# Performance work log

Measured on AMD Instinct MI355X. Metric: run time of the kernel, lower is better.

## Reference

```python
import jax, jax.numpy as jnp
import numpy as np

EPS = 1e-5

def group_norm(x, gamma, beta, groups):
    b, c, h, w = x.shape
    xg = x.reshape(b, groups, c // groups, h, w)
    mean = xg.mean(axis=(2, 3, 4), keepdims=True)
    var = xg.var(axis=(2, 3, 4), keepdims=True)
    xg = (xg - mean) * jax.lax.rsqrt(var + EPS)
    x = xg.reshape(b, c, h, w)
    return x * gamma[None, :, None, None] + beta[None, :, None, None]

def setup_inputs() -> dict:
    key = jax.random.key(0)
    ks = jax.random.split(key, 7)
    b, c, h, w = 8, 256, 64, 64
    x = jax.random.normal(ks[0], (b, c, h, w), dtype=jnp.float32)
    # GroupNorm affine params
    gamma = jnp.ones((c,), dtype=jnp.float32)
    beta = jnp.zeros((c,), dtype=jnp.float32)
    # 1x1 convs == linear maps over channel dim
    s = 1.0 / np.sqrt(c)
    w_qkv = jax.random.uniform(ks[1], (3 * c, c), jnp.float32, -s, s)
    b_qkv = jax.random.uniform(ks[2], (3 * c,), jnp.float32, -s, s)
    w_proj = jax.random.uniform(ks[3], (c, c), jnp.float32, -s, s)
    b_proj = jax.random.uniform(ks[4], (c,), jnp.float32, -s, s)
    return {"x": x, "gamma": gamma, "beta": beta, "w_qkv": w_qkv,
            "b_qkv": b_qkv, "w_proj": w_proj, "b_proj": b_proj}

def reference(x, gamma, beta, w_qkv, b_qkv, w_proj, b_proj):
    b, c, h, w = x.shape
    n = h * w
    h_in = x
    xn = group_norm(x, gamma, beta, groups=8)
    # 1x1 conv qkv: [b,c,h,w] -> [b,3c,h,w] -> [b,3c,n]
    qkv = jnp.einsum('oc,bchw->bohw', w_qkv, xn) + b_qkv[None, :, None, None]
    qkv = qkv.reshape(b, 3 * c, n)
    q, k, v = jnp.split(qkv, 3, axis=1)          # each [b,c,n]
    # attn = softmax(q^T k / sqrt(c)) over last dim
    scores = jnp.einsum('bci,bcj->bij', q, k) / jnp.sqrt(jnp.float32(c))
    attn = jax.nn.softmax(scores, axis=-1)       # [b,n,n]
    out = jnp.einsum('bij,bcj->bci', attn, v)    # [b,c,n]
    out = out.reshape(b, c, h, w)
    out = jnp.einsum('oc,bchw->bohw', w_proj, out) + b_proj[None, :, None, None]
    return h_in + out
```

## Files before the change

kernel.cpp:

```cpp
#include <hip/hip_runtime.h>
#include <hip/hip_bf16.h>
#include <stdint.h>

typedef __bf16 bf16_t;
typedef __bf16 bf16x8 __attribute__((ext_vector_type(8)));
typedef __bf16 bf16x4 __attribute__((ext_vector_type(4)));
typedef float f32x4 __attribute__((ext_vector_type(4)));
typedef float f32x16 __attribute__((ext_vector_type(16)));

#define NPIX 4096
#define CH 256

__global__ __launch_bounds__(256) void gn_partial_k(const float* __restrict__ x,
                                                    float* __restrict__ acc2) {
  int bg = blockIdx.x >> 3;
  int chunk = blockIdx.x & 7;
  const float4* xp = (const float4*)(x + (size_t)bg * 32 * NPIX) + chunk * (32 * NPIX / 4 / 8);
  float s = 0.f, ss = 0.f;
  for (int i = threadIdx.x; i < 32 * NPIX / 4 / 8; i += 256) {
    float4 v = xp[i];
    s  += v.x + v.y + v.z + v.w;
    ss += v.x * v.x + v.y * v.y + v.z * v.z + v.w * v.w;
  }
  int l = threadIdx.x & 63, w = threadIdx.x >> 6;
  #pragma unroll
  for (int off = 32; off; off >>= 1) { s += __shfl_down(s, off); ss += __shfl_down(ss, off); }
  __shared__ float rs[4], rss[4];
  if (l == 0) { rs[w] = s; rss[w] = ss; }
  __syncthreads();
  if (threadIdx.x == 0) {
    atomicAdd(&acc2[bg * 2],     rs[0] + rs[1] + rs[2] + rs[3]);
    atomicAdd(&acc2[bg * 2 + 1], rss[0] + rss[1] + rss[2] + rss[3]);
  }
}

__global__ void gn_finalize_k(const float* __restrict__ acc2, float* __restrict__ stats) {
  int bg = threadIdx.x;
  float mean = acc2[bg * 2] * (1.f / (32.f * NPIX));
  float var  = acc2[bg * 2 + 1] * (1.f / (32.f * NPIX)) - mean * mean;
  stats[bg * 2]     = mean;
  stats[bg * 2 + 1] = rsqrtf(var + 1e-5f);
}

__global__ __launch_bounds__(256) void gn_apply_t_k(const float* __restrict__ x,
    const float* __restrict__ stats, const float* __restrict__ gamma,
    const float* __restrict__ beta, bf16_t* __restrict__ xnT) {
  __shared__ float tile[32][33];
  int b = blockIdx.z;
  int p0 = blockIdx.x * 32, c0 = blockIdx.y * 32;
  int g = c0 >> 5;
  float mean = stats[(b * 8 + g) * 2], rstd = stats[(b * 8 + g) * 2 + 1];
  int tx = threadIdx.x, ty = threadIdx.y;
  const float* xb = x + ((size_t)b * CH + c0) * NPIX + p0;
  #pragma unroll
  for (int j = 0; j < 4; ++j) {
    int c = ty + j * 8;
    float v = xb[(size_t)c * NPIX + tx];
    tile[c][tx] = (v - mean) * rstd * gamma[c0 + c] + beta[c0 + c];
  }
  __syncthreads();
  bf16_t* op = xnT + ((size_t)b * NPIX + p0) * CH + c0;
  #pragma unroll
  for (int j = 0; j < 4; ++j) {
    int p = ty + j * 8;
    op[(size_t)p * CH + tx] = (bf16_t)tile[tx][p];
  }
}

__global__ __launch_bounds__(256) void cast_w_k(const float* __restrict__ wq,
    const float* __restrict__ wp, bf16_t* __restrict__ wqb, bf16_t* __restrict__ wpb) {
  int i = blockIdx.x * 256 + threadIdx.x;
  if (i < 768 * 256) wqb[i] = (bf16_t)wq[i];
  if (i < 256 * 256) wpb[i] = (bf16_t)wp[i];
}

#define LSTR 80

template <int MODE>
__global__ __launch_bounds__(256) void gemm_nt_k(
    const bf16_t* __restrict__ Ag, const bf16_t* __restrict__ Bg,
    int lda, int ldb, int K,
    void* __restrict__ O0, void* __restrict__ O1,
    const float* __restrict__ bias, const float* __restrict__ resid) {
  __shared__ __align__(16) char ldsA[128 * LSTR];
  __shared__ __align__(16) char ldsB[128 * LSTR];

  const int t = threadIdx.x;
  const int l = t & 63;
  const int w = t >> 6;
  const int wr = w >> 1, wc = w & 1;
  const int bm = blockIdx.x * 128;
  const int bn = blockIdx.y * 128;
  const int bz = blockIdx.z;

  const bf16_t* Ap = Ag;
  const bf16_t* Bp = Bg;
  if constexpr (MODE == 0) Ap += (size_t)bz * NPIX * CH;
  if constexpr (MODE == 3) Bp += (size_t)bz * NPIX * CH;

  f32x4 acc[4][4] = {};

  const int srow = t >> 2;
  const int scol = (t & 3) * 8;

  for (int k0 = 0; k0 < K; k0 += 32) {
    __syncthreads();
    #pragma unroll
    for (int it = 0; it < 2; ++it) {
      int r = it * 64 + srow;
      *(bf16x8*)(ldsA + r * LSTR + scol * 2) =
          *(const bf16x8*)(Ap + (size_t)(bm + r) * lda + k0 + scol);
      *(bf16x8*)(ldsB + r * LSTR + scol * 2) =
          *(const bf16x8*)(Bp + (size_t)(bn + r) * ldb + k0 + scol);
    }
    __syncthreads();
    bf16x8 fa[4], fb[4];
    #pragma unroll
    for (int m = 0; m < 4; ++m)
      fa[m] = *(const bf16x8*)(ldsA + (wr * 64 + m * 16 + (l & 15)) * LSTR + (l >> 4) * 16);
    #pragma unroll
    for (int n = 0; n < 4; ++n)
      fb[n] = *(const bf16x8*)(ldsB + (wc * 64 + n * 16 + (l & 15)) * LSTR + (l >> 4) * 16);
    #pragma unroll
    for (int m = 0; m < 4; ++m)
      #pragma unroll
      for (int n = 0; n < 4; ++n)
        acc[m][n] = __builtin_amdgcn_mfma_f32_16x16x32_bf16(fa[m], fb[n], acc[m][n], 0, 0, 0);
  }

  const int r0 = bm + wr * 64 + (l >> 4) * 4;
  const int c0 = bn + wc * 64 + (l & 15);
  #pragma unroll
  for (int m = 0; m < 4; ++m) {
    #pragma unroll
    for (int n = 0; n < 4; ++n) {
      int col = c0 + n * 16;
      #pragma unroll
      for (int j = 0; j < 4; ++j) {
        int row = r0 + m * 16 + j;
        float v = acc[m][n][j];
        if constexpr (MODE == 0) {
          float val = v + bias[col];
          if (col < 512)
            ((bf16_t*)O0)[(size_t)bz * NPIX * 512 + (size_t)row * 512 + col] = (bf16_t)val;
          else
            ((bf16_t*)O1)[(size_t)bz * CH * NPIX + (size_t)(col - 512) * NPIX + row] = (bf16_t)val;
        } else {
          size_t idx = (size_t)bz * CH * NPIX + (size_t)row * NPIX + col;
          ((float*)O0)[idx] = v + bias[row] + resid[idx];
        }
      }
    }
  }
}

#define KVB 64
#define KBYTES 32768
#define VBYTES 32768

__device__ __forceinline__ void dma16(const void* g, void* l) {
  __builtin_amdgcn_global_load_lds(
      (const __attribute__((address_space(1))) unsigned int*)g,
      (__attribute__((address_space(3))) unsigned int*)l, 16, 0, 0);
}

__device__ inline unsigned int pack2bf(float lo, float hi) {
  unsigned short a = __builtin_bit_cast(unsigned short, (bf16_t)lo);
  unsigned short b = __builtin_bit_cast(unsigned short, (bf16_t)hi);
  return (unsigned int)a | ((unsigned int)b << 16);
}

__global__ __launch_bounds__(512, 2) void flash_k(
    const bf16_t* __restrict__ qkT, const bf16_t* __restrict__ vglob,
    bf16_t* __restrict__ OT) {
  __shared__ __align__(16) char kS[2 * KBYTES];
  __shared__ __align__(16) char vS[2 * VBYTES];
  __shared__ float mls[8][2][32];

  const int t = threadIdx.x;
  const int l = t & 63, w = t >> 6;
  const int lq = l & 31, h = l >> 5;
  const int g = w >> 1, half = w & 1;
  const int batch = blockIdx.x & 7;
  const int q0 = (blockIdx.x >> 3) * 128;

  const bf16_t* qk_b = qkT + (size_t)batch * NPIX * 512;
  const bf16_t* v_b  = vglob + (size_t)batch * CH * NPIX;

  bf16x8 qf[16];
  const bf16_t* qrow = qk_b + (size_t)(q0 + g * 32 + lq) * 512 + h * 8;
  #pragma unroll
  for (int kk = 0; kk < 16; ++kk) qf[kk] = *(const bf16x8*)(qrow + kk * 16);

  const int krow_l = w * 8 + (l >> 5);
  const int kslot  = l & 31;
  const int vrow_l = w * 32 + (l >> 3);
  const int vslot  = l & 7;
  const bf16_t* ksrc = qk_b + 256;

  auto stage = [&](int tile, int buf) {
    #pragma unroll
    for (int it = 0; it < 4; ++it) {
      int r = krow_l + it * 2;
      dma16(ksrc + (size_t)(tile * KVB + r) * 512 + ((kslot ^ (r & 31)) << 3),
            kS + buf * KBYTES + (w * 8 + it * 2) * 512);
      int c = vrow_l + it * 8;
      dma16(v_b + (size_t)c * NPIX + tile * KVB + ((vslot ^ (c & 7)) << 3),
            vS + buf * VBYTES + (w * 32 + it * 8) * 128);
    }
  };

  stage(0, 0);
  __syncthreads();

  f32x16 acc_o[8] = {};
  float m = -1e30f, lsum = 0.f;
  const float c1 = 0.09016844006f;
  const int krow = half * 32 + lq;

  for (int tile = 0; tile < 64; ++tile) {
    const int cur = tile & 1;
    if (tile < 63) stage(tile + 1, cur ^ 1);

    f32x16 s = {};
    const char* kbase = kS + cur * KBYTES + krow * 512;
    #pragma unroll
    for (int kk = 0; kk < 16; ++kk) {
      bf16x8 kf = *(const bf16x8*)(kbase + (((2 * kk + h) ^ lq) << 4));
      s = __builtin_amdgcn_mfma_f32_32x32x16_bf16(kf, qf[kk], s, 0, 0, 0);
    }

    float tmax = -1e30f;
    #pragma unroll
    for (int r = 0; r < 16; ++r) { s[r] *= c1; tmax = fmaxf(tmax, s[r]); }
    tmax = fmaxf(tmax, __shfl_xor(tmax, 32, 64));
    if (!__all(tmax <= m + 10.f)) {
      float mnew = fmaxf(m, tmax);
      float sc = exp2f(m - mnew);
      m = mnew; lsum *= sc;
      #pragma unroll
      for (int n2 = 0; n2 < 8; ++n2)
        #pragma unroll
        for (int r = 0; r < 16; ++r) acc_o[n2][r] *= sc;
    }
    float ls = 0.f;
    #pragma unroll
    for (int r = 0; r < 16; ++r) { float p = exp2f(s[r] - m); s[r] = p; ls += p; }
    ls += __shfl_xor(ls, 32, 64);
    lsum += ls;

    bf16x8 pa[2];
    #pragma unroll
    for (int kk2 = 0; kk2 < 2; ++kk2) {
      const int hi = kk2 * 8;
      unsigned int wkeep[2], wsend[2];
      #pragma unroll
      for (int j = 0; j < 2; ++j) {
        float a0 = s[2 * j + hi],     b0 = s[2 * j + 1 + hi];
        float a1 = s[2 * j + 4 + hi], b1 = s[2 * j + 5 + hi];
        float ka = h ? a1 : a0, kb = h ? b1 : b0;
        float sa = h ? a0 : a1, sb = h ? b0 : b1;
        wkeep[j] = pack2bf(ka, kb);
        wsend[j] = pack2bf(sa, sb);
      }
      unsigned int wr0 = __shfl_xor(wsend[0], 32, 64);
      unsigned int wr1 = __shfl_xor(wsend[1], 32, 64);
      union { unsigned int u[4]; bf16x8 v; } pu;
      pu.u[0] = h ? wr0 : wkeep[0];
      pu.u[1] = h ? wr1 : wkeep[1];
      pu.u[2] = h ? wkeep[0] : wr0;
      pu.u[3] = h ? wkeep[1] : wr1;
      pa[kk2] = pu.v;
    }

    const char* vbase = vS + cur * VBYTES;
    #pragma unroll
    for (int n2 = 0; n2 < 8; ++n2) {
      const int vr = n2 * 32 + lq;
      #pragma unroll
      for (int kk2 = 0; kk2 < 2; ++kk2) {
        bf16x8 vf = *(const bf16x8*)(vbase + vr * 128 +
                     (((4 * half + 2 * kk2 + h) ^ (lq & 7)) << 4));
        acc_o[n2] = __builtin_amdgcn_mfma_f32_32x32x16_bf16(pa[kk2], vf, acc_o[n2], 0, 0, 0);
      }
    }
    __syncthreads();
  }

  if (h == 0) { mls[w][0][lq] = m; mls[w][1][lq] = lsum; }
  char* abuf = (g < 2) ? (kS + g * 32768) : (vS + (g - 2) * 32768);
  if (half == 1) {
    float* ab = (float*)abuf + l * 128;
    #pragma unroll
    for (int n2 = 0; n2 < 8; ++n2)
      #pragma unroll
      for (int q4 = 0; q4 < 4; ++q4) {
        f32x4 vv;
        vv[0] = acc_o[n2][q4 * 4 + 0]; vv[1] = acc_o[n2][q4 * 4 + 1];
        vv[2] = acc_o[n2][q4 * 4 + 2]; vv[3] = acc_o[n2][q4 * 4 + 3];
        *(f32x4*)(ab + n2 * 16 + q4 * 4) = vv;
      }
  }
  __syncthreads();
  if (half == 0) {
    float mB = mls[w + 1][0][lq], lB = mls[w + 1][1][lq];
    float mS = fmaxf(m, mB);
    float sA = exp2f(m - mS), sB = exp2f(mB - mS);
    float inv = 1.f / (lsum * sA + lB * sB);
    const float* ab = (const float*)abuf + l * 128;
    bf16_t* obase = OT + (size_t)batch * NPIX * CH + (size_t)(q0 + g * 32) * CH + lq;
    #pragma unroll
    for (int r = 0; r < 16; ++r) {
      int q = (r & 3) + 8 * (r >> 2) + 4 * h;
      float sAr = __shfl(sA, q, 64);
      float sBr = __shfl(sB, q, 64);
      float ivr = __shfl(inv, q, 64);
      bf16_t* orow = obase + (size_t)q * CH;
      #pragma unroll
      for (int n2 = 0; n2 < 8; ++n2) {
        float ob = (acc_o[n2][r] * sAr + ab[n2 * 16 + r] * sBr) * ivr;
        orow[n2 * 32] = (bf16_t)ob;
      }
    }
  }
}

extern "C" void kernel_launch(void* const* d_in, const int* in_sizes, int n_in,
                              void* d_out, int out_size, void* d_ws, size_t ws_size,
                              hipStream_t stream) {
  const float* x      = (const float*)d_in[0];
  const float* gamma  = (const float*)d_in[1];
  const float* beta   = (const float*)d_in[2];
  const float* w_qkv  = (const float*)d_in[3];
  const float* b_qkv  = (const float*)d_in[4];
  const float* w_proj = (const float*)d_in[5];
  const float* b_proj = (const float*)d_in[6];

  char* p = (char*)d_ws;
  auto alloc = [&](size_t bytes) {
    char* r = p;
    p += (bytes + 255) & ~(size_t)255;
    return (void*)r;
  };
  bf16_t* qkT  = (bf16_t*)alloc((size_t)8 * NPIX * 512 * 2);
  bf16_t* vbuf = (bf16_t*)alloc((size_t)8 * CH * NPIX * 2);
  bf16_t* OT   = (bf16_t*)alloc((size_t)8 * NPIX * CH * 2);
  bf16_t* wqb  = (bf16_t*)alloc(768 * 256 * 2);
  bf16_t* wpb  = (bf16_t*)alloc(256 * 256 * 2);
  float*  acc2 = (float*)alloc(64 * 2 * 4);
  float*  stats= (float*)alloc(64 * 2 * 4);
  bf16_t* xnT  = (bf16_t*)d_out;

  hipMemsetAsync(acc2, 0, 64 * 2 * 4, stream);
  gn_partial_k<<<64 * 8, 256, 0, stream>>>(x, acc2);
  gn_finalize_k<<<1, 64, 0, stream>>>(acc2, stats);
  gn_apply_t_k<<<dim3(128, 8, 8), dim3(32, 8), 0, stream>>>(x, stats, gamma, beta, xnT);
  cast_w_k<<<768, 256, 0, stream>>>(w_qkv, w_proj, wqb, wpb);

  gemm_nt_k<0><<<dim3(32, 6, 8), 256, 0, stream>>>(xnT, wqb, CH, CH, CH,
                                                   qkT, vbuf, b_qkv, nullptr);
  flash_k<<<256, 512, 0, stream>>>(qkT, vbuf, OT);

  gemm_nt_k<3><<<dim3(2, 32, 8), 256, 0, stream>>>(wpb, OT, CH, CH, CH,
                                                   d_out, nullptr, b_proj, x);
}
```

Baseline: 353.0 us.

## Software-pipeline flash attention: overlap PV of previous tile with softmax of current

Restructures the flash attention loop so the P·V MFMAs for the previous tile run while the softmax of the current tile is computed. V gets triple buffering and K drops to a single buffer reloaded after a mid-loop barrier. The softmax scale is folded into the Q projection epilogue, and s_setprio hints are added around the MFMA blocks. The aim is to hide exp/shuffle latency behind matrix work, at the cost of an extra barrier per tile and more registers for the carried P fragments.

New measurement: 428.8 us. 1.21x slower.

```diff
diff --git a/kernel.cpp b/kernel.cpp
--- a/kernel.cpp
+++ b/kernel.cpp
@@ -141,6 +141,7 @@
         float v = acc[m][n][j];
         if constexpr (MODE == 0) {
           float val = v + bias[col];
+          if (col < 256) val *= 0.09016844006f;
           if (col < 512)
             ((bf16_t*)O0)[(size_t)bz * NPIX * 512 + (size_t)row * 512 + col] = (bf16_t)val;
           else
@@ -173,8 +174,8 @@
 __global__ __launch_bounds__(512, 2) void flash_k(
     const bf16_t* __restrict__ qkT, const bf16_t* __restrict__ vglob,
     bf16_t* __restrict__ OT) {
-  __shared__ __align__(16) char kS[2 * KBYTES];
-  __shared__ __align__(16) char vS[2 * VBYTES];
+  __shared__ __align__(16) char kS[KBYTES];
+  __shared__ __align__(16) char vS[3 * VBYTES];
   __shared__ float mls[8][2][32];
 
   const int t = threadIdx.x;
@@ -198,58 +199,82 @@
   const int vslot  = l & 7;
   const bf16_t* ksrc = qk_b + 256;
 
-  auto stage = [&](int tile, int buf) {
+  auto stage_k = [&](int tile) {
     #pragma unroll
     for (int it = 0; it < 4; ++it) {
       int r = krow_l + it * 2;
       dma16(ksrc + (size_t)(tile * KVB + r) * 512 + ((kslot ^ (r & 31)) << 3),
-            kS + buf * KBYTES + (w * 8 + it * 2) * 512);
+            kS + (w * 8 + it * 2) * 512);
+    }
+  };
+  auto stage_v = [&](int tile, int slot) {
+    #pragma unroll
+    for (int it = 0; it < 4; ++it) {
       int c = vrow_l + it * 8;
       dma16(v_b + (size_t)c * NPIX + tile * KVB + ((vslot ^ (c & 7)) << 3),
-            vS + buf * VBYTES + (w * 32 + it * 8) * 128);
+            vS + slot * VBYTES + (w * 32 + it * 8) * 128);
     }
   };
 
-  stage(0, 0);
+  stage_k(0);
+  stage_v(0, 0);
   __syncthreads();
 
   f32x16 acc_o[8] = {};
   float m = -1e30f, lsum = 0.f;
-  const float c1 = 0.09016844006f;
   const int krow = half * 32 + lq;
+  const char* kbase = kS + krow * 512;
+  const int kxor = (h << 4) ^ (lq << 4);
+  const int vxor = (half << 6) ^ (h << 4) ^ ((lq & 7) << 4);
+  const char* vlane = vS + lq * 128;
+
+  bf16x8 paA[2];
+
+  auto pv = [&](int slot) {
+    const char* vb = vlane + slot * VBYTES;
+    __builtin_amdgcn_s_setprio(1);
+    #pragma unroll
+    for (int kk2 = 0; kk2 < 2; ++kk2) {
+      const char* vp = vb + (vxor ^ (kk2 << 5));
+      #pragma unroll
+      for (int n2 = 0; n2 < 8; ++n2) {
+        bf16x8 vf = *(const bf16x8*)(vp + n2 * 4096);
+        acc_o[n2] = __builtin_amdgcn_mfma_f32_32x32x16_bf16(paA[kk2], vf, acc_o[n2], 0, 0, 0);
+      }
+    }
+    __builtin_amdgcn_s_setprio(0);
+  };
 
   for (int tile = 0; tile < 64; ++tile) {
-    const int cur = tile & 1;
-    if (tile < 63) stage(tile + 1, cur ^ 1);
+    if (tile < 63) stage_v(tile + 1, (tile + 1) % 3);
 
     f32x16 s = {};
-    const char* kbase = kS + cur * KBYTES + krow * 512;
+    __builtin_amdgcn_s_setprio(1);
     #pragma unroll
     for (int kk = 0; kk < 16; ++kk) {
-      bf16x8 kf = *(const bf16x8*)(kbase + (((2 * kk + h) ^ lq) << 4));
+      bf16x8 kf = *(const bf16x8*)(kbase + (kxor ^ (kk << 5)));
       s = __builtin_amdgcn_mfma_f32_32x32x16_bf16(kf, qf[kk], s, 0, 0, 0);
     }
-
-    float tmax = -1e30f;
-    #pragma unroll
-    for (int r = 0; r < 16; ++r) { s[r] *= c1; tmax = fmaxf(tmax, s[r]); }
+    __builtin_amdgcn_s_setprio(0);
+    __syncthreads();
+    if (tile < 63) stage_k(tile + 1);
+
+    float tmax = s[0];
+    #pragma unroll
+    for (int r = 1; r < 16; ++r) tmax = fmaxf(tmax, s[r]);
     tmax = fmaxf(tmax, __shfl_xor(tmax, 32, 64));
-    if (!__all(tmax <= m + 10.f)) {
-      float mnew = fmaxf(m, tmax);
-      float sc = exp2f(m - mnew);
-      m = mnew; lsum *= sc;
-      #pragma unroll
-      for (int n2 = 0; n2 < 8; ++n2)
-        #pragma unroll
-        for (int r = 0; r < 16; ++r) acc_o[n2][r] *= sc;
-    }
+    const bool need = !__all(tmax <= m + 10.f);
+    float mnew = m, sc = 1.f;
+    if (need) { mnew = fmaxf(m, tmax); sc = exp2f(m - mnew); }
+
+    if (tile > 0) pv((tile + 2) % 3);
+
     float ls = 0.f;
     #pragma unroll
-    for (int r = 0; r < 16; ++r) { float p = exp2f(s[r] - m); s[r] = p; ls += p; }
+    for (int r = 0; r < 16; ++r) { float p = exp2f(s[r] - mnew); s[r] = p; ls += p; }
     ls += __shfl_xor(ls, 32, 64);
-    lsum += ls;
-
-    bf16x8 pa[2];
+
+    bf16x8 paB[2];
     #pragma unroll
     for (int kk2 = 0; kk2 < 2; ++kk2) {
       const int hi = kk2 * 8;
@@ -270,25 +295,26 @@
       pu.u[1] = h ? wr1 : wkeep[1];
       pu.u[2] = h ? wkeep[0] : wr0;
       pu.u[3] = h ? wkeep[1] : wr1;
-      pa[kk2] = pu.v;
-    }
-
-    const char* vbase = vS + cur * VBYTES;
-    #pragma unroll
-    for (int n2 = 0; n2 < 8; ++n2) {
-      const int vr = n2 * 32 + lq;
-      #pragma unroll
-      for (int kk2 = 0; kk2 < 2; ++kk2) {
-        bf16x8 vf = *(const bf16x8*)(vbase + vr * 128 +
-                     (((4 * half + 2 * kk2 + h) ^ (lq & 7)) << 4));
-        acc_o[n2] = __builtin_amdgcn_mfma_f32_32x32x16_bf16(pa[kk2], vf, acc_o[n2], 0, 0, 0);
-      }
-    }
+      paB[kk2] = pu.v;
+    }
+
+    if (need) {
+      #pragma unroll
+      for (int n2 = 0; n2 < 8; ++n2)
+        #pragma unroll
+        for (int r = 0; r < 16; ++r) acc_o[n2][r] *= sc;
+    }
+    lsum = lsum * sc + ls;
+    m = mnew;
+    paA[0] = paB[0]; paA[1] = paB[1];
+
     __syncthreads();
   }
+  pv(0);
+  __syncthreads();
 
   if (h == 0) { mls[w][0][lq] = m; mls[w][1][lq] = lsum; }
-  char* abuf = (g < 2) ? (kS + g * 32768) : (vS + (g - 2) * 32768);
+  char* abuf = (g == 0) ? kS : (vS + (g - 1) * VBYTES);
   if (half == 1) {
     float* ab = (float*)abuf + l * 128;
     #pragma unroll
```
